# Kernel optimization log

Hardware: AMD Instinct MI355X
Metric: run time of the kernel (lower is better)

Reference implementation:

```python
import jax, jax.numpy as jnp
import numpy as np

N = 50000
IN_CH = 128
HEADS = 4
OUT_CH = 16
HID = HEADS * OUT_CH  # 64
E = 800000
B_EXP = 2.0
EPS = 1e-06
LN_EPS = 1e-05

def _l2norm(v, axis):
    n = jnp.sqrt(jnp.sum(v * v, axis=axis, keepdims=True))
    return v / jnp.maximum(n, 1e-12)  # matches F.normalize eps

def setup_inputs() -> dict:
    key = jax.random.key(0)
    k1, k2, k3, k4 = jax.random.split(key, 4)
    x = jax.random.normal(k1, (N, IN_CH), dtype=jnp.float32)
    edge_index = jax.random.randint(k2, (2, E), 0, N, dtype=jnp.int64)
    # lin: xavier_uniform over [HID, IN_CH]
    bound = float(np.sqrt(6.0 / (HID + IN_CH)))
    lin_w = jax.random.uniform(k3, (HID, IN_CH), dtype=jnp.float32, minval=-bound, maxval=bound)
    bcos_w = jax.random.normal(k4, (HID, HID), dtype=jnp.float32) * (1.0 / np.sqrt(HID))
    ln_gamma = jnp.ones((HID,), dtype=jnp.float32)
    ln_beta = jnp.zeros((HID,), dtype=jnp.float32)
    return {"x": x, "edge_index": edge_index, "lin_w": lin_w,
            "bcos_w": bcos_w, "ln_gamma": ln_gamma, "ln_beta": ln_beta}

def reference(x, edge_index, lin_w, bcos_w, ln_gamma, ln_beta):
    row, col = edge_index[0], edge_index[1]
    h = (x @ lin_w.T).reshape(N, HEADS, OUT_CH)          # [N,H,D]
    h_norm = _l2norm(h, axis=2)
    # per-edge cosine between source (col) and target (row) node features
    cos = jnp.sum(h_norm[col] * h_norm[row], axis=2)     # [E,H]
    cos = jnp.clip(cos, EPS, 1.0)
    scale = cos ** (B_EXP - 1.0)                         # [E,H]
    messages = h[col] * scale[:, :, None]                # [E,H,D]
    # scatter-add messages to target nodes
    out = jax.ops.segment_sum(messages.reshape(E, HID), row, num_segments=N)  # [N,HID]
    # BcosLinearNoBias
    lin = out @ bcos_w.T
    o_n = _l2norm(out, axis=1)
    w_n = _l2norm(bcos_w, axis=1)
    cos2 = jnp.clip(o_n @ w_n.T, EPS, 1.0)
    out_bcos = lin * cos2 ** (B_EXP - 1.0)
    # LayerNorm
    mu = jnp.mean(out_bcos, axis=-1, keepdims=True)
    var = jnp.mean((out_bcos - mu) ** 2, axis=-1, keepdims=True)
    out_norm = (out_bcos - mu) / jnp.sqrt(var + LN_EPS) * ln_gamma + ln_beta
    # dropout is identity in eval mode
    return out_norm
```

## Files before the change

### kernel.cpp

```cpp
#include <hip/hip_runtime.h>
#include <math.h>

#define N_NODES 50000
#define IN_CH   128
#define HEADS   4
#define HID     64
#define NEDGE   800000
#define EPS     1e-6f
#define LN_EPS  1e-5f
#define PAD     48
#define MTILES  (N_NODES / 16)

typedef __attribute__((ext_vector_type(8))) _Float16 f16x8;
typedef __attribute__((ext_vector_type(4))) float    f32x4;

#define DPP_ADD_F(p, ctrl) \
    p += __int_as_float(__builtin_amdgcn_update_dpp(0, __float_as_int(p), ctrl, 0xF, 0xF, true))
#define REDUCE16_DPP(p) { DPP_ADD_F(p,0xB1); DPP_ADD_F(p,0x4E); \
                          DPP_ADD_F(p,0x141); DPP_ADD_F(p,0x140); }
#define REDUCE4_DPP(p)  { DPP_ADD_F(p,0xB1); DPP_ADD_F(p,0x4E); }
#define REDUCE64(p) { REDUCE16_DPP(p); p += __shfl_xor(p,16); p += __shfl_xor(p,32); }

__global__ __launch_bounds__(256, 4) void h_kernel(const float* __restrict__ x,
                                                   const float* __restrict__ lin_w,
                                                   float* __restrict__ h,
                                                   float* __restrict__ inv_hn,
                                                   const int* __restrict__ ei,
                                                   int* __restrict__ deg,
                                                   int* __restrict__ csr_col) {
    int lane = threadIdx.x & 63;
    int wave = threadIdx.x >> 6;

    int t = blockIdx.x * 256 + threadIdx.x;
    bool have_e = (t < NEDGE / 4);
    int4 r, c;
    if (have_e) {
        r = ((const int4*)ei)[t];
        c = ((const int4*)(ei + NEDGE))[t];
    }
    int k0, k1, k2, k3;
    if (have_e) {
        k0 = atomicAdd(&deg[r.x], 1);
        k1 = atomicAdd(&deg[r.y], 1);
        k2 = atomicAdd(&deg[r.z], 1);
        k3 = atomicAdd(&deg[r.w], 1);
    }

    int mt = blockIdx.x * 4 + wave;
    if (mt < MTILES) {
        int node0 = mt * 16;
        int mrow  = lane & 15;
        int kg    = lane >> 4;
        const float4* xp = (const float4*)x;
        const float4* w4 = (const float4*)lin_w;

        f16x8 A[4];
#pragma unroll
        for (int s = 0; s < 4; ++s) {
            float4 u0 = xp[(node0 + mrow) * 32 + s * 8 + kg * 2];
            float4 u1 = xp[(node0 + mrow) * 32 + s * 8 + kg * 2 + 1];
            f16x8 a;
            a[0] = (_Float16)u0.x; a[1] = (_Float16)u0.y;
            a[2] = (_Float16)u0.z; a[3] = (_Float16)u0.w;
            a[4] = (_Float16)u1.x; a[5] = (_Float16)u1.y;
            a[6] = (_Float16)u1.z; a[7] = (_Float16)u1.w;
            A[s] = a;
        }

#pragma unroll
        for (int nt = 0; nt < 4; ++nt) {
            f32x4 C = {0.f, 0.f, 0.f, 0.f};
#pragma unroll
            for (int s = 0; s < 4; ++s) {
                int wrow = nt * 16 + mrow;
                float4 u0 = w4[wrow * 32 + s * 8 + kg * 2];
                float4 u1 = w4[wrow * 32 + s * 8 + kg * 2 + 1];
                f16x8 b;
                b[0] = (_Float16)u0.x; b[1] = (_Float16)u0.y;
                b[2] = (_Float16)u0.z; b[3] = (_Float16)u0.w;
                b[4] = (_Float16)u1.x; b[5] = (_Float16)u1.y;
                b[6] = (_Float16)u1.z; b[7] = (_Float16)u1.w;
                C = __builtin_amdgcn_mfma_f32_16x16x32_f16(A[s], b, C, 0, 0, 0);
            }
            float ss0 = C[0] * C[0], ss1 = C[1] * C[1];
            float ss2 = C[2] * C[2], ss3 = C[3] * C[3];
#pragma unroll
            for (int rr = 0; rr < 4; ++rr)
                h[(node0 + 4 * kg + rr) * HID + nt * 16 + mrow] = C[rr];
            REDUCE16_DPP(ss0); REDUCE16_DPP(ss1);
            REDUCE16_DPP(ss2); REDUCE16_DPP(ss3);
            if (mrow == 0) {
                inv_hn[(node0 + 4 * kg + 0) * HEADS + nt] = 1.0f / fmaxf(sqrtf(ss0), 1e-12f);
                inv_hn[(node0 + 4 * kg + 1) * HEADS + nt] = 1.0f / fmaxf(sqrtf(ss1), 1e-12f);
                inv_hn[(node0 + 4 * kg + 2) * HEADS + nt] = 1.0f / fmaxf(sqrtf(ss2), 1e-12f);
                inv_hn[(node0 + 4 * kg + 3) * HEADS + nt] = 1.0f / fmaxf(sqrtf(ss3), 1e-12f);
            }
        }
    }

    if (have_e) {
        if (k0 < PAD) __builtin_nontemporal_store(c.x, &csr_col[r.x * PAD + k0]);
        if (k1 < PAD) __builtin_nontemporal_store(c.y, &csr_col[r.y * PAD + k1]);
        if (k2 < PAD) __builtin_nontemporal_store(c.z, &csr_col[r.z * PAD + k2]);
        if (k3 < PAD) __builtin_nontemporal_store(c.w, &csr_col[r.w * PAD + k3]);
    }
}

__global__ __launch_bounds__(256, 4) void gather_final(const int* __restrict__ deg,
                                                       const int* __restrict__ csr_col,
                                                       const float* __restrict__ h,
                                                       const float* __restrict__ inv_hn,
                                                       const float* __restrict__ bcos_w,
                                                       const float* __restrict__ gamma,
                                                       const float* __restrict__ beta,
                                                       float* __restrict__ y) {
    __shared__ float4 wt4[16][65];
    __shared__ float rowbuf[4][HID];
    __shared__ float ivw[HID], gm[HID], bt[HID];

    for (int i = threadIdx.x; i < HID * (HID / 4); i += 256) {
        int j = i >> 4, k4 = i & 15;
        wt4[k4][j] = ((const float4*)bcos_w)[i];
    }
    if (threadIdx.x < HID) {
        gm[threadIdx.x] = gamma[threadIdx.x];
        bt[threadIdx.x] = beta[threadIdx.x];
    }
    __syncthreads();
    if (threadIdx.x < HID) {
        float ss = 0.f;
#pragma unroll
        for (int k4 = 0; k4 < 16; ++k4) {
            float4 q = wt4[k4][threadIdx.x];
            ss += q.x * q.x + q.y * q.y + q.z * q.z + q.w * q.w;
        }
        ivw[threadIdx.x] = 1.0f / fmaxf(sqrtf(ss), 1e-12f);
    }
    __syncthreads();

    int grp    = threadIdx.x >> 6;
    int lane   = threadIdx.x & 63;
    int e_slot = lane >> 4;
    int ch4    = lane & 15;
    int hd     = ch4 >> 2;

    const float4* h4 = (const float4*)h;

    for (int g = blockIdx.x; g < N_NODES / 4; g += gridDim.x) {
        int node = g * 4 + grp;
        float4 hq  = h4[node * 16 + ch4];
        float  ihr = inv_hn[node * HEADS + hd];
        float4 hrs4 = make_float4(hq.x * ihr, hq.y * ihr, hq.z * ihr, hq.w * ihr);
        int dg    = __builtin_amdgcn_readfirstlane(min(deg[node], PAD));
        int start = node * PAD;

        float4 acc = make_float4(0.f, 0.f, 0.f, 0.f);
#pragma unroll 1
        for (int bb = 0; bb < dg; bb += 16) {
            int   cc[4];
            float4 hh[4];
            float ii[4];
#pragma unroll
            for (int s = 0; s < 4; ++s) {
                int e = bb + s * 4 + e_slot;
                int ix = (e < dg) ? e : dg - 1;
                cc[s] = csr_col[start + ix];
            }
#pragma unroll
            for (int s = 0; s < 4; ++s) hh[s] = h4[cc[s] * 16 + ch4];
#pragma unroll
            for (int s = 0; s < 4; ++s) ii[s] = inv_hn[cc[s] * HEADS + hd];
#pragma unroll
            for (int s = 0; s < 4; ++s) {
                float p = hh[s].x * hrs4.x + hh[s].y * hrs4.y
                        + hh[s].z * hrs4.z + hh[s].w * hrs4.w;
                REDUCE4_DPP(p);
                float sc = fminf(fmaxf(p * ii[s], EPS), 1.0f);
                int e = bb + s * 4 + e_slot;
                sc = (e < dg) ? sc : 0.0f;
                acc.x = fmaf(hh[s].x, sc, acc.x);
                acc.y = fmaf(hh[s].y, sc, acc.y);
                acc.z = fmaf(hh[s].z, sc, acc.z);
                acc.w = fmaf(hh[s].w, sc, acc.w);
            }
        }
        acc.x += __shfl_xor(acc.x, 16); acc.x += __shfl_xor(acc.x, 32);
        acc.y += __shfl_xor(acc.y, 16); acc.y += __shfl_xor(acc.y, 32);
        acc.z += __shfl_xor(acc.z, 16); acc.z += __shfl_xor(acc.z, 32);
        acc.w += __shfl_xor(acc.w, 16); acc.w += __shfl_xor(acc.w, 32);

        if (lane < 16) ((float4*)rowbuf[grp])[ch4] = acc;
        float o = rowbuf[grp][lane];

        float ss = o * o;
        REDUCE64(ss);
        float inv_no = 1.0f / fmaxf(sqrtf(ss), 1e-12f);

        const float4* rb4 = (const float4*)rowbuf[grp];
        float lin = 0.f;
#pragma unroll
        for (int k4 = 0; k4 < 16; ++k4) {
            float4 a  = rb4[k4];
            float4 wv = wt4[k4][lane];
            lin += a.x * wv.x + a.y * wv.y + a.z * wv.z + a.w * wv.w;
        }

        float c2v = lin * inv_no * ivw[lane];
        c2v = fminf(fmaxf(c2v, EPS), 1.0f);
        float ob = lin * c2v;

        float mu = ob;
        REDUCE64(mu);
        mu *= (1.0f / 64.0f);
        float d = ob - mu;
        float var = d * d;
        REDUCE64(var);
        var *= (1.0f / 64.0f);
        float r = rsqrtf(var + LN_EPS);
        y[node * HID + lane] = d * r * gm[lane] + bt[lane];
    }
}

extern "C" void kernel_launch(void* const* d_in, const int* in_sizes, int n_in,
                              void* d_out, int out_size, void* d_ws, size_t ws_size,
                              hipStream_t stream) {
    const float* x      = (const float*)d_in[0];
    const int*   ei     = (const int*)d_in[1];
    const float* lin_w  = (const float*)d_in[2];
    const float* bcos_w = (const float*)d_in[3];
    const float* gamma  = (const float*)d_in[4];
    const float* beta   = (const float*)d_in[5];
    float*       y      = (float*)d_out;

    float* h       = (float*)d_ws;
    float* inv_hn  = h + (size_t)N_NODES * HID;
    int*   deg     = (int*)(inv_hn + (size_t)N_NODES * HEADS);
    int*   csr_col = deg + N_NODES;

    const int H_BLOCKS = (MTILES + 3) / 4;

    hipMemsetAsync(deg, 0, N_NODES * sizeof(int), stream);

    h_kernel<<<H_BLOCKS, 256, 0, stream>>>(x, lin_w, h, inv_hn, ei, deg, csr_col);

    gather_final<<<2048, 256, 0, stream>>>(deg, csr_col, h, inv_hn,
                                           bcos_w, gamma, beta, y);
}
```

Before: 126.2 us.

## Build padded CSR with segmented LDS counting instead of global atomics

Replaces the global atomicAdd-based degree counting, previously fused into the projection kernel, with a three-kernel segmented counting sort. Per-segment byte-packed counts go into shared memory, are prefix-summed across segments, and are then used to place edges deterministically. The projection kernel no longer handles edges. This removes contended global atomics but adds two extra launches and extra passes over the edge list. It also reuses the h workspace region for the counts and relies on 8-bit counters, which limits per-node degree to 255.

```diff
diff --git a/kernel.cpp b/kernel.cpp
--- a/kernel.cpp
+++ b/kernel.cpp
@@ -10,6 +10,9 @@
 #define LN_EPS  1e-5f
 #define PAD     48
 #define MTILES  (N_NODES / 16)
+#define SEGS    100
+#define SEG     8000
+#define NG      12500
 
 typedef __attribute__((ext_vector_type(8))) _Float16 f16x8;
 typedef __attribute__((ext_vector_type(4))) float    f32x4;
@@ -21,92 +24,134 @@
 #define REDUCE4_DPP(p)  { DPP_ADD_F(p,0xB1); DPP_ADD_F(p,0x4E); }
 #define REDUCE64(p) { REDUCE16_DPP(p); p += __shfl_xor(p,16); p += __shfl_xor(p,32); }
 
+__global__ __launch_bounds__(512) void cnt_kernel(const int* __restrict__ ei,
+                                                  unsigned* __restrict__ cnt,
+                                                  unsigned char* __restrict__ lrank) {
+    __shared__ unsigned lc[NG];
+    for (int i = threadIdx.x; i < NG; i += 512) lc[i] = 0u;
+    __syncthreads();
+    int base = blockIdx.x * SEG;
+#pragma unroll 1
+    for (int it = 0; it < SEG / 512 + 1; ++it) {
+        int el = it * 512 + threadIdx.x;
+        if (el < SEG) {
+            int e = base + el;
+            int n = ei[e];
+            unsigned sh  = 8u * (n & 3);
+            unsigned old = atomicAdd(&lc[n >> 2], 1u << sh);
+            lrank[e] = (unsigned char)((old >> sh) & 0xFFu);
+        }
+    }
+    __syncthreads();
+    for (int i = threadIdx.x; i < NG; i += 512)
+        cnt[blockIdx.x * NG + i] = lc[i];
+}
+
+__global__ __launch_bounds__(256) void prefix_kernel(unsigned* __restrict__ cnt,
+                                                     unsigned* __restrict__ deg4) {
+    int g = blockIdx.x * 256 + threadIdx.x;
+    if (g >= NG) return;
+    unsigned run = 0u;
+#pragma unroll 1
+    for (int s = 0; s < SEGS; s += 4) {
+        unsigned c0 = cnt[(s + 0) * NG + g];
+        unsigned c1 = cnt[(s + 1) * NG + g];
+        unsigned c2 = cnt[(s + 2) * NG + g];
+        unsigned c3 = cnt[(s + 3) * NG + g];
+        cnt[(s + 0) * NG + g] = run; run += c0;
+        cnt[(s + 1) * NG + g] = run; run += c1;
+        cnt[(s + 2) * NG + g] = run; run += c2;
+        cnt[(s + 3) * NG + g] = run; run += c3;
+    }
+    deg4[g] = run;
+}
+
+__global__ __launch_bounds__(256) void fill_kernel(const int* __restrict__ ei,
+                                                   const unsigned* __restrict__ sbase,
+                                                   const unsigned char* __restrict__ lrank,
+                                                   int* __restrict__ csr_col) {
+    int t = blockIdx.x * 256 + threadIdx.x;
+    if (t >= NEDGE / 4) return;
+    int s = t / (SEG / 4);
+    int4 r = ((const int4*)ei)[t];
+    int4 c = ((const int4*)(ei + NEDGE))[t];
+    unsigned lr4 = ((const unsigned*)lrank)[t];
+
+    int n0 = r.x, n1 = r.y, n2 = r.z, n3 = r.w;
+    int sb0 = (sbase[s * NG + (n0 >> 2)] >> (8 * (n0 & 3))) & 0xFF;
+    int sb1 = (sbase[s * NG + (n1 >> 2)] >> (8 * (n1 & 3))) & 0xFF;
+    int sb2 = (sbase[s * NG + (n2 >> 2)] >> (8 * (n2 & 3))) & 0xFF;
+    int sb3 = (sbase[s * NG + (n3 >> 2)] >> (8 * (n3 & 3))) & 0xFF;
+    int sl0 = sb0 + ((lr4 >> 0)  & 0xFF);
+    int sl1 = sb1 + ((lr4 >> 8)  & 0xFF);
+    int sl2 = sb2 + ((lr4 >> 16) & 0xFF);
+    int sl3 = sb3 + ((lr4 >> 24) & 0xFF);
+    if (sl0 < PAD) __builtin_nontemporal_store(c.x, &csr_col[n0 * PAD + sl0]);
+    if (sl1 < PAD) __builtin_nontemporal_store(c.y, &csr_col[n1 * PAD + sl1]);
+    if (sl2 < PAD) __builtin_nontemporal_store(c.z, &csr_col[n2 * PAD + sl2]);
+    if (sl3 < PAD) __builtin_nontemporal_store(c.w, &csr_col[n3 * PAD + sl3]);
+}
+
 __global__ __launch_bounds__(256, 4) void h_kernel(const float* __restrict__ x,
                                                    const float* __restrict__ lin_w,
                                                    float* __restrict__ h,
-                                                   float* __restrict__ inv_hn,
-                                                   const int* __restrict__ ei,
-                                                   int* __restrict__ deg,
-                                                   int* __restrict__ csr_col) {
+                                                   float* __restrict__ inv_hn) {
     int lane = threadIdx.x & 63;
     int wave = threadIdx.x >> 6;
-
-    int t = blockIdx.x * 256 + threadIdx.x;
-    bool have_e = (t < NEDGE / 4);
-    int4 r, c;
-    if (have_e) {
-        r = ((const int4*)ei)[t];
-        c = ((const int4*)(ei + NEDGE))[t];
-    }
-    int k0, k1, k2, k3;
-    if (have_e) {
-        k0 = atomicAdd(&deg[r.x], 1);
-        k1 = atomicAdd(&deg[r.y], 1);
-        k2 = atomicAdd(&deg[r.z], 1);
-        k3 = atomicAdd(&deg[r.w], 1);
-    }
-
     int mt = blockIdx.x * 4 + wave;
-    if (mt < MTILES) {
-        int node0 = mt * 16;
-        int mrow  = lane & 15;
-        int kg    = lane >> 4;
-        const float4* xp = (const float4*)x;
-        const float4* w4 = (const float4*)lin_w;
-
-        f16x8 A[4];
+    if (mt >= MTILES) return;
+
+    int node0 = mt * 16;
+    int mrow  = lane & 15;
+    int kg    = lane >> 4;
+    const float4* xp = (const float4*)x;
+    const float4* w4 = (const float4*)lin_w;
+
+    f16x8 A[4];
+#pragma unroll
+    for (int s = 0; s < 4; ++s) {
+        float4 u0 = xp[(node0 + mrow) * 32 + s * 8 + kg * 2];
+        float4 u1 = xp[(node0 + mrow) * 32 + s * 8 + kg * 2 + 1];
+        f16x8 a;
+        a[0] = (_Float16)u0.x; a[1] = (_Float16)u0.y;
+        a[2] = (_Float16)u0.z; a[3] = (_Float16)u0.w;
+        a[4] = (_Float16)u1.x; a[5] = (_Float16)u1.y;
+        a[6] = (_Float16)u1.z; a[7] = (_Float16)u1.w;
+        A[s] = a;
+    }
+
+#pragma unroll
+    for (int nt = 0; nt < 4; ++nt) {
+        f32x4 C = {0.f, 0.f, 0.f, 0.f};
 #pragma unroll
         for (int s = 0; s < 4; ++s) {
-            float4 u0 = xp[(node0 + mrow) * 32 + s * 8 + kg * 2];
-            float4 u1 = xp[(node0 + mrow) * 32 + s * 8 + kg * 2 + 1];
-            f16x8 a;
-            a[0] = (_Float16)u0.x; a[1] = (_Float16)u0.y;
-            a[2] = (_Float16)u0.z; a[3] = (_Float16)u0.w;
-            a[4] = (_Float16)u1.x; a[5] = (_Float16)u1.y;
-            a[6] = (_Float16)u1.z; a[7] = (_Float16)u1.w;
-            A[s] = a;
-        }
-
-#pragma unroll
-        for (int nt = 0; nt < 4; ++nt) {
-            f32x4 C = {0.f, 0.f, 0.f, 0.f};
-#pragma unroll
-            for (int s = 0; s < 4; ++s) {
-                int wrow = nt * 16 + mrow;
-                float4 u0 = w4[wrow * 32 + s * 8 + kg * 2];
-                float4 u1 = w4[wrow * 32 + s * 8 + kg * 2 + 1];
-                f16x8 b;
-                b[0] = (_Float16)u0.x; b[1] = (_Float16)u0.y;
-                b[2] = (_Float16)u0.z; b[3] = (_Float16)u0.w;
-                b[4] = (_Float16)u1.x; b[5] = (_Float16)u1.y;
-                b[6] = (_Float16)u1.z; b[7] = (_Float16)u1.w;
-                C = __builtin_amdgcn_mfma_f32_16x16x32_f16(A[s], b, C, 0, 0, 0);
-            }
-            float ss0 = C[0] * C[0], ss1 = C[1] * C[1];
-            float ss2 = C[2] * C[2], ss3 = C[3] * C[3];
-#pragma unroll
-            for (int rr = 0; rr < 4; ++rr)
-                h[(node0 + 4 * kg + rr) * HID + nt * 16 + mrow] = C[rr];
-            REDUCE16_DPP(ss0); REDUCE16_DPP(ss1);
-            REDUCE16_DPP(ss2); REDUCE16_DPP(ss3);
-            if (mrow == 0) {
-                inv_hn[(node0 + 4 * kg + 0) * HEADS + nt] = 1.0f / fmaxf(sqrtf(ss0), 1e-12f);
-                inv_hn[(node0 + 4 * kg + 1) * HEADS + nt] = 1.0f / fmaxf(sqrtf(ss1), 1e-12f);
-                inv_hn[(node0 + 4 * kg + 2) * HEADS + nt] = 1.0f / fmaxf(sqrtf(ss2), 1e-12f);
-                inv_hn[(node0 + 4 * kg + 3) * HEADS + nt] = 1.0f / fmaxf(sqrtf(ss3), 1e-12f);
-            }
-        }
-    }
-
-    if (have_e) {
-        if (k0 < PAD) __builtin_nontemporal_store(c.x, &csr_col[r.x * PAD + k0]);
-        if (k1 < PAD) __builtin_nontemporal_store(c.y, &csr_col[r.y * PAD + k1]);
-        if (k2 < PAD) __builtin_nontemporal_store(c.z, &csr_col[r.z * PAD + k2]);
-        if (k3 < PAD) __builtin_nontemporal_store(c.w, &csr_col[r.w * PAD + k3]);
-    }
-}
-
-__global__ __launch_bounds__(256, 4) void gather_final(const int* __restrict__ deg,
+            int wrow = nt * 16 + mrow;
+            float4 u0 = w4[wrow * 32 + s * 8 + kg * 2];
+            float4 u1 = w4[wrow * 32 + s * 8 + kg * 2 + 1];
+            f16x8 b;
+            b[0] = (_Float16)u0.x; b[1] = (_Float16)u0.y;
+            b[2] = (_Float16)u0.z; b[3] = (_Float16)u0.w;
+            b[4] = (_Float16)u1.x; b[5] = (_Float16)u1.y;
+            b[6] = (_Float16)u1.z; b[7] = (_Float16)u1.w;
+            C = __builtin_amdgcn_mfma_f32_16x16x32_f16(A[s], b, C, 0, 0, 0);
+        }
+        float ss0 = C[0] * C[0], ss1 = C[1] * C[1];
+        float ss2 = C[2] * C[2], ss3 = C[3] * C[3];
+#pragma unroll
+        for (int rr = 0; rr < 4; ++rr)
+            h[(node0 + 4 * kg + rr) * HID + nt * 16 + mrow] = C[rr];
+        REDUCE16_DPP(ss0); REDUCE16_DPP(ss1);
+        REDUCE16_DPP(ss2); REDUCE16_DPP(ss3);
+        if (mrow == 0) {
+            inv_hn[(node0 + 4 * kg + 0) * HEADS + nt] = 1.0f / fmaxf(sqrtf(ss0), 1e-12f);
+            inv_hn[(node0 + 4 * kg + 1) * HEADS + nt] = 1.0f / fmaxf(sqrtf(ss1), 1e-12f);
+            inv_hn[(node0 + 4 * kg + 2) * HEADS + nt] = 1.0f / fmaxf(sqrtf(ss2), 1e-12f);
+            inv_hn[(node0 + 4 * kg + 3) * HEADS + nt] = 1.0f / fmaxf(sqrtf(ss3), 1e-12f);
+        }
+    }
+}
+
+__global__ __launch_bounds__(256, 4) void gather_final(const unsigned char* __restrict__ deg8,
                                                        const int* __restrict__ csr_col,
                                                        const float* __restrict__ h,
                                                        const float* __restrict__ inv_hn,
@@ -151,7 +196,7 @@
         float4 hq  = h4[node * 16 + ch4];
         float  ihr = inv_hn[node * HEADS + hd];
         float4 hrs4 = make_float4(hq.x * ihr, hq.y * ihr, hq.z * ihr, hq.w * ihr);
-        int dg    = __builtin_amdgcn_readfirstlane(min(deg[node], PAD));
+        int dg    = __builtin_amdgcn_readfirstlane(min((int)deg8[node], PAD));
         int start = node * PAD;
 
         float4 acc = make_float4(0.f, 0.f, 0.f, 0.f);
@@ -232,17 +277,21 @@
     const float* beta   = (const float*)d_in[5];
     float*       y      = (float*)d_out;
 
-    float* h       = (float*)d_ws;
-    float* inv_hn  = h + (size_t)N_NODES * HID;
-    int*   deg     = (int*)(inv_hn + (size_t)N_NODES * HEADS);
-    int*   csr_col = deg + N_NODES;
-
-    const int H_BLOCKS = (MTILES + 3) / 4;
-
-    hipMemsetAsync(deg, 0, N_NODES * sizeof(int), stream);
-
-    h_kernel<<<H_BLOCKS, 256, 0, stream>>>(x, lin_w, h, inv_hn, ei, deg, csr_col);
-
-    gather_final<<<2048, 256, 0, stream>>>(deg, csr_col, h, inv_hn,
-                                           bcos_w, gamma, beta, y);
-}
+    float* h        = (float*)d_ws;
+    unsigned* cnt   = (unsigned*)d_ws;
+    unsigned char* lrank = (unsigned char*)d_ws + (size_t)SEGS * NG * 4;
+    float* inv_hn   = h + (size_t)N_NODES * HID;
+    unsigned* deg4  = (unsigned*)(inv_hn + (size_t)N_NODES * HEADS);
+    int*   csr_col  = (int*)(deg4 + NG);
+
+    cnt_kernel<<<SEGS, 512, 0, stream>>>(ei, cnt, lrank);
+
+    prefix_kernel<<<(NG + 255) / 256, 256, 0, stream>>>(cnt, deg4);
+
+    fill_kernel<<<(NEDGE / 4 + 255) / 256, 256, 0, stream>>>(ei, cnt, lrank, csr_col);
+
+    h_kernel<<<(MTILES + 3) / 4, 256, 0, stream>>>(x, lin_w, h, inv_hn);
+
+    gather_final<<<2048, 256, 0, stream>>>((const unsigned char*)deg4, csr_col,
+                                           h, inv_hn, bcos_w, gamma, beta, y);
+}
```

New measurement: 128.8 us. 2.1% more time.
